# Performance work log

Measured on AMD Instinct MI355X. Metric: run time of the kernel, lower is better.

Reference implementation:

```python
import jax, jax.numpy as jnp
import numpy as np

N_NODES = 50000
N_EDGES = 600000
D = 128  # input_nf = output_nf = hidden_nf
EDGE_IN = 2 * D + 1   # source, target, radial
NODE_IN = 2 * D       # x, agg


def _glorot(key, shape):
    fan_in, fan_out = shape[0], shape[1]
    lim = float(np.sqrt(6.0 / (fan_in + fan_out)))
    return jax.random.uniform(key, shape, jnp.float32, -lim, lim)


def setup_inputs() -> dict:
    key = jax.random.key(0)
    ks = jax.random.split(key, 16)
    h = jax.random.normal(ks[0], (N_NODES, D), jnp.float32)
    edge_index = jax.random.randint(ks[1], (2, N_EDGES), 0, N_NODES, jnp.int64 if jax.config.read('jax_enable_x64') else jnp.int32)
    coord = jax.random.uniform(ks[2], (N_NODES, 3), jnp.float32)
    l = jnp.array([10.0, 10.0, 10.0], jnp.float32)  # periodic box lengths (non-trainable buffer)
    return {
        'h': h, 'edge_index': edge_index, 'coord': coord, 'num_nodes': N_NODES, 'l': l,
        # edge_mlp: Linear(257,128) SiLU Linear(128,128) SiLU
        'We1': _glorot(ks[3], (EDGE_IN, D)), 'be1': jnp.zeros((D,), jnp.float32),
        'We2': _glorot(ks[4], (D, D)),       'be2': jnp.zeros((D,), jnp.float32),
        # node_mlp: Linear(256,128) SiLU Linear(128,128)
        'Wn1': _glorot(ks[5], (NODE_IN, D)), 'bn1': jnp.zeros((D,), jnp.float32),
        'Wn2': _glorot(ks[6], (D, D)),       'bn2': jnp.zeros((D,), jnp.float32),
        # coord_mlp: Linear(128,128) SiLU Linear(128,1, bias=False, xavier gain=0.001)
        'Wc1': _glorot(ks[7], (D, D)),       'bc1': jnp.zeros((D,), jnp.float32),
        'Wc2': _glorot(ks[8], (D, 1)) * 0.001,
    }


def reference(h, edge_index, coord, num_nodes, l,
              We1, be1, We2, be2, Wn1, bn1, Wn2, bn2, Wc1, bc1, Wc2):
    row, col = edge_index[0], edge_index[1]

    # coord2radial with periodic minimum-image wrap
    diff = coord[row] - coord[col]                       # [E, 3]
    diff = jnp.where(diff > 0.5 * l, diff - l, diff)
    diff = jnp.where(diff < -0.5 * l, diff + l, diff)
    radial = jnp.sum(diff * diff, axis=1, keepdims=True)  # [E, 1]

    # edge model: gather -> concat -> 2-layer SiLU MLP
    eh = jnp.concatenate([h[row], h[col], radial], axis=1)  # [E, 257]
    eh = jax.nn.silu(eh @ We1 + be1)
    edge_feat = jax.nn.silu(eh @ We2 + be2)                 # [E, 128]

    # coord model: trans/agg computed in the original but discarded (dead code);
    # only the periodic remainder of coord is returned.
    coord_out = jnp.remainder(coord, l)

    # node model: scatter-add edge features into nodes, then MLP + residual
    agg = jax.ops.segment_sum(edge_feat, row, num_segments=num_nodes)  # [N, 128]
    nh = jnp.concatenate([h, agg], axis=1)                              # [N, 256]
    nh = jax.nn.silu(nh @ Wn1 + bn1)
    h_out = h + (nh @ Wn2 + bn2)

    return h_out, coord_out, edge_feat
```

## Files before the change

### kernel.cpp

```cpp
#include <hip/hip_runtime.h>
#include <math.h>

#define D 128
#define SXS 264
#define SHS 132
#define SFS 132

typedef unsigned int u32;
typedef unsigned short u16;
typedef __attribute__((ext_vector_type(8))) short bf16x8;
typedef __attribute__((ext_vector_type(4))) float f32x4;
typedef __attribute__((ext_vector_type(2))) float f32x2;

__device__ __forceinline__ float bfl(u32 u) { return __uint_as_float(u << 16); }
__device__ __forceinline__ float bfh(u32 u) { return __uint_as_float(u & 0xFFFF0000u); }
__device__ __forceinline__ u16 f2bf(float f) {
    u32 u = __float_as_uint(f);
    return (u16)((u + 0x7FFFu + ((u >> 16) & 1u)) >> 16);
}
__device__ __forceinline__ u32 cvt_pk_bf16(float lo, float hi) {
    u32 r;
    asm("v_cvt_pk_bf16_f32 %0, %1, %2" : "=v"(r) : "v"(lo), "v"(hi));
    return r;
}
__device__ __forceinline__ u16 cvt1_bf16(float v) { return (u16)cvt_pk_bf16(v, v); }
__device__ __forceinline__ float silu_f(float x) {
    float e = __expf(-x);
    return x * __builtin_amdgcn_rcpf(1.0f + e);
}
__device__ __forceinline__ void atomic_pk_add_bf16(u16* addr, u32 pk) {
    asm volatile("global_atomic_pk_add_bf16 %0, %1, off sc1"
                 :: "v"(addr), "v"(pk) : "memory");
}

__global__ void coord_kernel(const float* __restrict__ coord,
                             const float* __restrict__ lbox,
                             float* __restrict__ out, int n3) {
    int i = blockIdx.x * 256 + threadIdx.x;
    if (i < n3) {
        float ld = lbox[i % 3];
        float c = coord[i];
        float r = fmodf(c, ld);
        if (r < 0.f) r += ld;
        out[i] = r;
    }
}

__global__ __launch_bounds__(256) void prep_plus_kernel(
    const float* __restrict__ We1, const float* __restrict__ We2,
    const float* __restrict__ Wn1, const float* __restrict__ Wn2,
    u16* __restrict__ wt,
    int* __restrict__ cursor, int N,
    u16* __restrict__ agg16, long agg_n,
    int* __restrict__ bstate,
    int B1, int B2, int B3)
{
    const int b = blockIdx.x, t = threadIdx.x;
    if (b < B1) {
        int i = b * 256 + t;
        if (i < 32768)        { int n = i >> 8, k = i & 255;              wt[i] = f2bf(We1[(size_t)k*D + n]); }
        else if (i < 49152)   { int j = i - 32768; int n = j >> 7, k = j & 127; wt[i] = f2bf(We2[(size_t)k*D + n]); }
        else if (i < 81920)   { int j = i - 49152; int n = j >> 8, k = j & 255; wt[i] = f2bf(Wn1[(size_t)k*D + n]); }
        else                  { int j = i - 81920; int n = j >> 7, k = j & 127; wt[i] = f2bf(Wn2[(size_t)k*D + n]); }
    } else if (b < B2) {
        int i = ((b - B1) * 256 + t) * 4;
        if (i + 3 < N) *(int4*)(cursor + i) = make_int4(0, 0, 0, 0);
        else for (int k = 0; k < 4; ++k) if (i + k < N) cursor[i + k] = 0;
    } else if (b < B3) {
        long i = ((long)(b - B2) * 256 + t) * 8;
        if (agg16 && i < agg_n) *(uint4*)(agg16 + i) = make_uint4(0, 0, 0, 0);
    } else {
        if (t < 64) bstate[t] = 0;
    }
}

__global__ void hist4_kernel(const int* __restrict__ ei, int* __restrict__ cnt, int E) {
    int i = (blockIdx.x * 256 + threadIdx.x) * 4;
    if (i + 3 < E) {
        int4 r = *(const int4*)(ei + i);
        atomicAdd(&cnt[r.x], 1); atomicAdd(&cnt[r.y], 1);
        atomicAdd(&cnt[r.z], 1); atomicAdd(&cnt[r.w], 1);
    } else {
        for (int k = 0; k < 4; ++k) if (i + k < E) atomicAdd(&cnt[ei[i + k]], 1);
    }
}

__global__ __launch_bounds__(256) void scan_lb_kernel(int* __restrict__ cursor,
                                                      int* __restrict__ bstate, int n) {
    __shared__ int s[256];
    __shared__ int sExcl;
    const int t = threadIdx.x, b = blockIdx.x;
    const int base = b * 1024 + t * 4;
    int v[4];
    #pragma unroll
    for (int i = 0; i < 4; ++i) { int idx = base + i; v[i] = (idx < n - 1) ? cursor[idx] : 0; }
    int lsum = v[0] + v[1] + v[2] + v[3];
    s[t] = lsum; __syncthreads();
    #pragma unroll
    for (int off = 1; off < 256; off <<= 1) {
        int x = (t >= off) ? s[t - off] : 0; __syncthreads();
        s[t] += x; __syncthreads();
    }
    if (t == 0)
        __hip_atomic_store(&bstate[b], 0x40000000 | s[255], __ATOMIC_RELEASE, __HIP_MEMORY_SCOPE_AGENT);
    if (t < 64) {
        int val = 0;
        if (t < b) {
            int st;
            do { st = __hip_atomic_load(&bstate[t], __ATOMIC_ACQUIRE, __HIP_MEMORY_SCOPE_AGENT); }
            while (!(st & 0x40000000));
            val = st & 0x3FFFFFFF;
        }
        #pragma unroll
        for (int off = 1; off < 64; off <<= 1) val += __shfl_xor(val, off, 64);
        if (t == 0) sExcl = val;
    }
    __syncthreads();
    int run = sExcl + s[t] - lsum;
    #pragma unroll
    for (int i = 0; i < 4; ++i) {
        int idx = base + i;
        if (idx < n - 1) cursor[idx] = run;
        run += v[i];
    }
}

__global__ void scan1_kernel(const int* __restrict__ cnt, int* __restrict__ offs,
                             int* __restrict__ bsum, int n) {
    __shared__ int s[256];
    int t = threadIdx.x, b = blockIdx.x;
    int base = b * 1024 + t * 4;
    int v[4];
    #pragma unroll
    for (int i = 0; i < 4; ++i) { int idx = base + i; v[i] = (idx < n - 1) ? cnt[idx] : 0; }
    int lsum = v[0] + v[1] + v[2] + v[3];
    s[t] = lsum; __syncthreads();
    #pragma unroll
    for (int off = 1; off < 256; off <<= 1) {
        int x = (t >= off) ? s[t - off] : 0; __syncthreads();
        s[t] += x; __syncthreads();
    }
    int run = s[t] - lsum;
    #pragma unroll
    for (int i = 0; i < 4; ++i) { int idx = base + i; if (idx < n) offs[idx] = run; run += v[i]; }
    if (t == 255) bsum[b] = s[255];
}

__global__ void scan2_kernel(int* __restrict__ bsum, int nb) {
    __shared__ int s[64];
    int t = threadIdx.x;
    int orig = (t < nb) ? bsum[t] : 0;
    s[t] = orig; __syncthreads();
    #pragma unroll
    for (int off = 1; off < 64; off <<= 1) {
        int x = (t >= off) ? s[t - off] : 0; __syncthreads();
        s[t] += x; __syncthreads();
    }
    if (t < nb) bsum[t] = s[t] - orig;
}

__global__ void scan3_kernel(int* __restrict__ offs, const int* __restrict__ bsum,
                             int* __restrict__ cursor, int n) {
    int i = blockIdx.x * 256 + threadIdx.x;
    if (i < n) {
        int v = offs[i] + bsum[i >> 10];
        offs[i] = v;
        if (i < n - 1) cursor[i] = v;
    }
}

__global__ void scatter4_kernel(const int* __restrict__ ei, int* __restrict__ cursor,
                                int* __restrict__ perm, int4* __restrict__ edata, int E) {
    int i = (blockIdx.x * 256 + threadIdx.x) * 4;
    if (i + 3 < E) {
        int4 r = *(const int4*)(ei + i);
        int4 c = *(const int4*)(ei + (size_t)E + i);
        int p0 = atomicAdd(&cursor[r.x], 1);
        int p1 = atomicAdd(&cursor[r.y], 1);
        int p2 = atomicAdd(&cursor[r.z], 1);
        int p3 = atomicAdd(&cursor[r.w], 1);
        if (edata) {
            edata[p0] = make_int4(i,     r.x, c.x, 0);
            edata[p1] = make_int4(i + 1, r.y, c.y, 0);
            edata[p2] = make_int4(i + 2, r.z, c.z, 0);
            edata[p3] = make_int4(i + 3, r.w, c.w, 0);
        } else {
            perm[p0] = i; perm[p1] = i + 1; perm[p2] = i + 2; perm[p3] = i + 3;
        }
    } else {
        for (int k = 0; k < 4; ++k) {
            int e = i + k;
            if (e < E) {
                int r = ei[e], c = ei[(size_t)E + e];
                int p = atomicAdd(&cursor[r], 1);
                if (edata) edata[p] = make_int4(e, r, c, 0);
                else perm[p] = e;
            }
        }
    }
}

__global__ __launch_bounds__(256, 4) void pq_kernel(
    const float* __restrict__ h, const u16* __restrict__ wt,
    const float* __restrict__ be1,
    u16* __restrict__ Pt, u16* __restrict__ Qt, int N,
    const float* __restrict__ coord, const float* __restrict__ lbox,
    float* __restrict__ coord_out, int n3, int NBn)
{
    __shared__ __align__(16) u16 sA[64 * SHS];
    __shared__ __align__(16) u16 sO[64 * SHS];

    const int t = threadIdx.x;

    if (blockIdx.x >= NBn) {
        int i = (blockIdx.x - NBn) * 256 + t;
        if (i < n3) {
            float ld = lbox[i % 3];
            float c = coord[i];
            float r = fmodf(c, ld);
            if (r < 0.f) r += ld;
            coord_out[i] = r;
        }
        return;
    }

    const int lane = t & 63;
    const int wid = t >> 6;
    const int n0 = blockIdx.x * 64;

    {
        const int e = t & 63, q = t >> 6;
        int ng = n0 + e; int ns = (ng < N) ? ng : N - 1;
        const float4* src = (const float4*)(h + (size_t)ns * D + q * 32);
        u16* dst = sA + e * SHS + q * 32;
        #pragma unroll
        for (int c = 0; c < 4; ++c) {
            float4 a = src[2 * c], b = src[2 * c + 1];
            *(uint4*)(dst + c * 8) = make_uint4(cvt_pk_bf16(a.x, a.y), cvt_pk_bf16(a.z, a.w),
                                               cvt_pk_bf16(b.x, b.y), cvt_pk_bf16(b.z, b.w));
        }
    }
    __syncthreads();

    const int lrow = lane & 15;
    const int kg = lane >> 4;
    const int g4 = kg * 4;
    const int nbase = wid * 32;

    f32x4 accP[4][2] = {}, accQ[4][2] = {};
    {
        bf16x8 Bt[8], Bm[8];
        #pragma unroll
        for (int nn = 0; nn < 2; ++nn)
            #pragma unroll
            for (int s = 0; s < 4; ++s) {
                const u16* bp = wt + (size_t)(nbase + nn * 16 + lrow) * 256 + s * 32 + kg * 8;
                Bt[nn * 4 + s] = *(const bf16x8*)bp;
                Bm[nn * 4 + s] = *(const bf16x8*)(bp + 128);
            }
        #pragma unroll
        for (int s = 0; s < 4; ++s) {
            bf16x8 a[4];
            #pragma unroll
            for (int m = 0; m < 4; ++m)
                a[m] = *(const bf16x8*)(sA + (m * 16 + lrow) * SHS + s * 32 + kg * 8);
            #pragma unroll
            for (int m = 0; m < 4; ++m)
                #pragma unroll
                for (int nn = 0; nn < 2; ++nn) {
                    accP[m][nn] = __builtin_amdgcn_mfma_f32_16x16x32_bf16(a[m], Bt[nn * 4 + s], accP[m][nn], 0, 0, 0);
                    accQ[m][nn] = __builtin_amdgcn_mfma_f32_16x16x32_bf16(a[m], Bm[nn * 4 + s], accQ[m][nn], 0, 0, 0);
                }
        }
    }

    #pragma unroll
    for (int nn = 0; nn < 2; ++nn) {
        int outc = nbase + nn * 16 + lrow;
        float bb = be1[outc];
        #pragma unroll
        for (int m = 0; m < 4; ++m)
            #pragma unroll
            for (int r = 0; r < 4; ++r)
                sO[(m * 16 + g4 + r) * SHS + outc] = cvt1_bf16(accP[m][nn][r] + bb);
    }
    __syncthreads();
    {
        const int f4 = t & 15, rb = t >> 4;
        #pragma unroll
        for (int p = 0; p < 4; ++p) {
            int row = rb + p * 16;
            int ng = n0 + row;
            if (ng < N)
                *(uint4*)(Pt + (size_t)ng * D + f4 * 8) = *(const uint4*)(sO + row * SHS + f4 * 8);
        }
    }
    __syncthreads();
    #pragma unroll
    for (int nn = 0; nn < 2; ++nn) {
        int outc = nbase + nn * 16 + lrow;
        #pragma unroll
        for (int m = 0; m < 4; ++m)
            #pragma unroll
            for (int r = 0; r < 4; ++r)
                sO[(m * 16 + g4 + r) * SHS + outc] = cvt1_bf16(accQ[m][nn][r]);
    }
    __syncthreads();
    {
        const int f4 = t & 15, rb = t >> 4;
        #pragma unroll
        for (int p = 0; p < 4; ++p) {
            int row = rb + p * 16;
            int ng = n0 + row;
            if (ng < N)
                *(uint4*)(Qt + (size_t)ng * D + f4 * 8) = *(const uint4*)(sO + row * SHS + f4 * 8);
        }
    }
}

__global__ __launch_bounds__(256, 8) void edge_pq_kernel(
    const u16* __restrict__ Pt, const u16* __restrict__ Qt,
    const int* __restrict__ ei, const int* __restrict__ perm,
    const int4* __restrict__ edata,
    const float* __restrict__ coord, const float* __restrict__ lbox,
    const u16* __restrict__ wt, const float* __restrict__ We1,
    const float* __restrict__ be2,
    float* __restrict__ ef_out, float* __restrict__ aggf,
    u16* __restrict__ agg16, int E)
{
    __shared__ __align__(16) u16 uni[64 * SHS];
    __shared__ int srow[64], scol[64], sEid[64];
    __shared__ float sRad[64];
    __shared__ float sW[128];
    u16* sH1 = uni;
    u16* sE16 = uni;

    const int t = threadIdx.x;
    const int lane = t & 63;
    const int wid = t >> 6;

    int p0;
    {
        const int nwg = gridDim.x;
        const int orig = blockIdx.x;
        const int q = nwg >> 3, r = nwg & 7;
        const int xcd = orig & 7, idx = orig >> 3;
        const int tile = (xcd < r ? xcd * (q + 1) : r * (q + 1) + (xcd - r) * q) + idx;
        p0 = tile * 64;
    }

    if (t < 64) {
        int slot = p0 + t;
        bool valid = slot < E;
        int cs = valid ? slot : (E - 1);
        int eg, rr, cc;
        if (edata) {
            int4 ed = edata[cs];
            eg = ed.x; rr = ed.y; cc = ed.z;
        } else {
            eg = perm[cs];
            rr = ei[eg];
            cc = ei[(size_t)E + eg];
        }
        sEid[t] = valid ? eg : -1;
        srow[t] = rr;
        scol[t] = cc;
        float rad = 0.f;
        #pragma unroll
        for (int d3 = 0; d3 < 3; ++d3) {
            float df = coord[(size_t)rr * 3 + d3] - coord[(size_t)cc * 3 + d3];
            float ld = lbox[d3];
            df = (df >  0.5f * ld) ? df - ld : df;
            df = (df < -0.5f * ld) ? df + ld : df;
            rad += df * df;
        }
        sRad[t] = rad;
    } else if (t < 192) {
        sW[t - 64] = We1[(size_t)256 * D + (t - 64)];
    }
    __syncthreads();

    {
        const int e = t & 63, q = t >> 6;
        const u16* Pp = Pt + (size_t)srow[e] * D;
        const u16* Qp = Qt + (size_t)scol[e] * D;
        const float rad = sRad[e];
        #pragma unroll
        for (int c0 = 0; c0 < 4; ++c0) {
            int j0 = q * 32 + c0 * 8;
            uint4 pu = *(const uint4*)(Pp + j0);
            uint4 qu = *(const uint4*)(Qp + j0);
            u32 pa[4] = {pu.x, pu.y, pu.z, pu.w};
            u32 qa[4] = {qu.x, qu.y, qu.z, qu.w};
            u32 ow[4];
            #pragma unroll
            for (int k = 0; k < 4; ++k) {
                float w0 = sW[j0 + 2 * k], w1 = sW[j0 + 2 * k + 1];
                float v0 = silu_f(bfl(pa[k]) + bfl(qa[k]) + rad * w0);
                float v1 = silu_f(bfh(pa[k]) + bfh(qa[k]) + rad * w1);
                ow[k] = cvt_pk_bf16(v0, v1);
            }
            *(uint4*)(sH1 + e * SHS + j0) = make_uint4(ow[0], ow[1], ow[2], ow[3]);
        }
    }
    __syncthreads();

    const int lrow = lane & 15;
    const int kg = lane >> 4;
    const int g4 = kg * 4;
    const int nbase = wid * 32;

    f32x4 acc2[4][2] = {};
    {
        bf16x8 B2[8];
        #pragma unroll
        for (int nn = 0; nn < 2; ++nn)
            #pragma unroll
            for (int s = 0; s < 4; ++s)
                B2[nn * 4 + s] = *(const bf16x8*)(wt + 32768 + (size_t)(nbase + nn * 16 + lrow) * 128 + s * 32 + kg * 8);
        #pragma unroll
        for (int s = 0; s < 4; ++s) {
            bf16x8 a[4];
            #pragma unroll
            for (int m = 0; m < 4; ++m)
                a[m] = *(const bf16x8*)(sH1 + (m * 16 + lrow) * SHS + s * 32 + kg * 8);
            #pragma unroll
            for (int m = 0; m < 4; ++m)
                #pragma unroll
                for (int nn = 0; nn < 2; ++nn)
                    acc2[m][nn] = __builtin_amdgcn_mfma_f32_16x16x32_bf16(a[m], B2[nn * 4 + s], acc2[m][nn], 0, 0, 0);
        }
    }
    __syncthreads();

    #pragma unroll
    for (int nn = 0; nn < 2; ++nn) {
        int outc = nbase + nn * 16 + lrow;
        float bb = be2[outc];
        #pragma unroll
        for (int m = 0; m < 4; ++m)
            #pragma unroll
            for (int r = 0; r < 4; ++r)
                sE16[(m * 16 + g4 + r) * SHS + outc] = cvt1_bf16(silu_f(acc2[m][nn][r] + bb));
    }
    __syncthreads();

    if (agg16) {
        const int cp = t & 63;
        const int g = t >> 6;
        const int ebeg = g * 16, eend = ebeg + 16;
        float r0 = 0.f, r1 = 0.f;
        int prev = srow[ebeg];
        for (int e = ebeg; e < eend; ++e) {
            int r = srow[e];
            if (r != prev) {
                if (r0 != 0.f || r1 != 0.f)
                    atomic_pk_add_bf16(agg16 + (size_t)prev * D + 2 * cp, cvt_pk_bf16(r0, r1));
                r0 = 0.f; r1 = 0.f; prev = r;
            }
            int eg = sEid[e];
            if (eg >= 0) {
                u32 pk2 = *(const u32*)(sE16 + e * SHS + 2 * cp);
                float v0 = bfl(pk2), v1 = bfh(pk2);
                f32x2 vv = {v0, v1};
                __builtin_nontemporal_store(vv, (f32x2*)&ef_out[(size_t)eg * D + 2 * cp]);
                r0 += v0; r1 += v1;
            }
        }
        if (r0 != 0.f || r1 != 0.f)
            atomic_pk_add_bf16(agg16 + (size_t)prev * D + 2 * cp, cvt_pk_bf16(r0, r1));
    } else {
        const int ct = t & 127;
        const int half = t >> 7;
        const int ebeg = half * 32, eend = ebeg + 32;
        float run = 0.f;
        int prev = srow[ebeg];
        for (int e = ebeg; e < eend; ++e) {
            int r = srow[e];
            if (r != prev) {
                if (run != 0.f) atomicAdd(&aggf[(size_t)prev * D + ct], run);
                run = 0.f; prev = r;
            }
            int eg = sEid[e];
            if (eg >= 0) {
                float v = __uint_as_float((u32)sE16[e * SHS + ct] << 16);
                __builtin_nontemporal_store(v, &ef_out[(size_t)eg * D + ct]);
                run += v;
            }
        }
        if (run != 0.f) atomicAdd(&aggf[(size_t)prev * D + ct], run);
    }
}

__global__ __launch_bounds__(256, 3) void edge_fb_kernel(
    const float* __restrict__ h,
    const int* __restrict__ ei, const int* __restrict__ perm,
    const float* __restrict__ coord, const float* __restrict__ lbox,
    const u16* __restrict__ wt,
    const float* __restrict__ We1, const float* __restrict__ be1,
    const float* __restrict__ be2,
    float* __restrict__ ef_out, float* __restrict__ aggf, int E)
{
    __shared__ __align__(16) u16 sX[64 * SXS];
    __shared__ __align__(16) u16 sH1[64 * SHS];
    __shared__ int srow[64], scol[64], sEid[64];
    __shared__ float sRad[64];

    const int t = threadIdx.x;
    const int lane = t & 63;
    const int wid = t >> 6;

    int p0;
    {
        const int nwg = gridDim.x;
        const int orig = blockIdx.x;
        const int q = nwg >> 3, r = nwg & 7;
        const int xcd = orig & 7, idx = orig >> 3;
        const int tile = (xcd < r ? xcd * (q + 1) : r * (q + 1) + (xcd - r) * q) + idx;
        p0 = tile * 64;
    }

    if (t < 64) {
        int slot = p0 + t;
        int eg = perm[(slot < E) ? slot : (E - 1)];
        sEid[t] = (p0 + t < E) ? eg : -1;
        srow[t] = ei[eg];
        scol[t] = ei[(size_t)E + eg];
    }
    __syncthreads();

    {
        const int e = t & 63;
        const int q = t >> 6;
        const int r = srow[e], c = scol[e];
        const float4* src = (const float4*)((q < 2) ? (h + (size_t)r * D + (q & 1) * 64)
                                                    : (h + (size_t)c * D + (q & 1) * 64));
        u16* dst = sX + e * SXS + q * 64;
        #pragma unroll
        for (int i = 0; i < 8; ++i) {
            float4 a = src[2 * i], b = src[2 * i + 1];
            *(uint4*)(dst + i * 8) = make_uint4(cvt_pk_bf16(a.x, a.y), cvt_pk_bf16(a.z, a.w),
                                               cvt_pk_bf16(b.x, b.y), cvt_pk_bf16(b.z, b.w));
        }
        if (t < 64) {
            int rr = srow[t], cc = scol[t];
            float rad = 0.f;
            #pragma unroll
            for (int d3 = 0; d3 < 3; ++d3) {
                float df = coord[(size_t)rr * 3 + d3] - coord[(size_t)cc * 3 + d3];
                float ld = lbox[d3];
                df = (df >  0.5f * ld) ? df - ld : df;
                df = (df < -0.5f * ld) ? df + ld : df;
                rad += df * df;
            }
            sRad[t] = rad;
        }
    }
    __syncthreads();

    const int lrow = lane & 15;
    const int kg = lane >> 4;
    const int g4 = kg * 4;
    const int nbase = wid * 32;

    f32x4 acc[4][2] = {};
    {
        bf16x8 B1[16];
        #pragma unroll
        for (int nn = 0; nn < 2; ++nn)
            #pragma unroll
            for (int s = 0; s < 8; ++s)
                B1[nn * 8 + s] = *(const bf16x8*)(wt + (size_t)(nbase + nn * 16 + lrow) * 256 + s * 32 + kg * 8);
        #pragma unroll
        for (int s = 0; s < 8; ++s) {
            bf16x8 a[4];
            #pragma unroll
            for (int m = 0; m < 4; ++m)
                a[m] = *(const bf16x8*)(sX + (m * 16 + lrow) * SXS + s * 32 + kg * 8);
            #pragma unroll
            for (int m = 0; m < 4; ++m)
                #pragma unroll
                for (int nn = 0; nn < 2; ++nn)
                    acc[m][nn] = __builtin_amdgcn_mfma_f32_16x16x32_bf16(a[m], B1[nn * 8 + s], acc[m][nn], 0, 0, 0);
        }
    }

    #pragma unroll
    for (int nn = 0; nn < 2; ++nn) {
        int outc = nbase + nn * 16 + lrow;
        float wl = We1[(size_t)256 * D + outc];
        float bb = be1[outc];
        #pragma unroll
        for (int m = 0; m < 4; ++m)
            #pragma unroll
            for (int r = 0; r < 4; ++r) {
                int e = m * 16 + g4 + r;
                float v = acc[m][nn][r] + sRad[e] * wl + bb;
                sH1[e * SHS + outc] = cvt1_bf16(silu_f(v));
            }
    }
    __syncthreads();

    f32x4 acc2[4][2] = {};
    {
        bf16x8 B2[8];
        #pragma unroll
        for (int nn = 0; nn < 2; ++nn)
            #pragma unroll
            for (int s = 0; s < 4; ++s)
                B2[nn * 4 + s] = *(const bf16x8*)(wt + 32768 + (size_t)(nbase + nn * 16 + lrow) * 128 + s * 32 + kg * 8);
        #pragma unroll
        for (int s = 0; s < 4; ++s) {
            bf16x8 a[4];
            #pragma unroll
            for (int m = 0; m < 4; ++m)
                a[m] = *(const bf16x8*)(sH1 + (m * 16 + lrow) * SHS + s * 32 + kg * 8);
            #pragma unroll
            for (int m = 0; m < 4; ++m)
                #pragma unroll
                for (int nn = 0; nn < 2; ++nn)
                    acc2[m][nn] = __builtin_amdgcn_mfma_f32_16x16x32_bf16(a[m], B2[nn * 4 + s], acc2[m][nn], 0, 0, 0);
        }
    }
    __syncthreads();

    float* sXf = (float*)sX;
    #pragma unroll
    for (int nn = 0; nn < 2; ++nn) {
        int outc = nbase + nn * 16 + lrow;
        float bb = be2[outc];
        #pragma unroll
        for (int m = 0; m < 4; ++m)
            #pragma unroll
            for (int r = 0; r < 4; ++r)
                sXf[(m * 16 + g4 + r) * SFS + outc] = silu_f(acc2[m][nn][r] + bb);
    }
    __syncthreads();

    {
        const int ct = t & 127;
        const int half = t >> 7;
        const int ebeg = half * 32, eend = ebeg + 32;
        float run = 0.f;
        int prev = srow[ebeg];
        for (int e = ebeg; e < eend; ++e) {
            int r = srow[e];
            if (r != prev) {
                if (run != 0.f) atomicAdd(&aggf[(size_t)prev * D + ct], run);
                run = 0.f; prev = r;
            }
            int eg = sEid[e];
            if (eg >= 0) {
                float v = sXf[e * SFS + ct];
                __builtin_nontemporal_store(v, &ef_out[(size_t)eg * D + ct]);
                run += v;
            }
        }
        if (run != 0.f) atomicAdd(&aggf[(size_t)prev * D + ct], run);
    }
}

__global__ __launch_bounds__(256, 4) void node_kernel(
    const float* __restrict__ h, const float* __restrict__ aggf,
    const u16* __restrict__ agg16,
    const u16* __restrict__ wt,
    const float* __restrict__ bn1, const float* __restrict__ bn2,
    float* __restrict__ h_out, int N)
{
    __shared__ __align__(16) u16 uni[64 * SXS];
    u16* sX = uni;
    u16* sH1 = uni;
    float* sXf = (float*)uni;

    const int t = threadIdx.x;
    const int lane = t & 63;
    const int wid = t >> 6;
    const int n0 = blockIdx.x * 64;

    {
        const int e = t & 63;
        const int q = t >> 6;
        int ng = n0 + e; int ns = (ng < N) ? ng : N - 1;
        u16* dst = sX + e * SXS + q * 64;
        if (q >= 2 && agg16) {
            const u16* src = agg16 + (size_t)ns * D + (q & 1) * 64;
            #pragma unroll
            for (int i = 0; i < 8; ++i)
                *(uint4*)(dst + i * 8) = *(const uint4*)(src + i * 8);
        } else {
            const float4* src = (const float4*)(((q < 2) ? h : aggf) + (size_t)ns * D + (q & 1) * 64);
            #pragma unroll
            for (int i = 0; i < 8; ++i) {
                float4 a = src[2 * i], b = src[2 * i + 1];
                *(uint4*)(dst + i * 8) = make_uint4(cvt_pk_bf16(a.x, a.y), cvt_pk_bf16(a.z, a.w),
                                                   cvt_pk_bf16(b.x, b.y), cvt_pk_bf16(b.z, b.w));
            }
        }
    }
    __syncthreads();

    const int lrow = lane & 15;
    const int kg = lane >> 4;
    const int g4 = kg * 4;
    const int nbase = wid * 32;

    f32x4 acc[4][2] = {};
    {
        bf16x8 B1[16];
        #pragma unroll
        for (int nn = 0; nn < 2; ++nn)
            #pragma unroll
            for (int s = 0; s < 8; ++s)
                B1[nn * 8 + s] = *(const bf16x8*)(wt + 49152 + (size_t)(nbase + nn * 16 + lrow) * 256 + s * 32 + kg * 8);
        #pragma unroll
        for (int s = 0; s < 8; ++s) {
            bf16x8 a[4];
            #pragma unroll
            for (int m = 0; m < 4; ++m)
                a[m] = *(const bf16x8*)(sX + (m * 16 + lrow) * SXS + s * 32 + kg * 8);
            #pragma unroll
            for (int m = 0; m < 4; ++m)
                #pragma unroll
                for (int nn = 0; nn < 2; ++nn)
                    acc[m][nn] = __builtin_amdgcn_mfma_f32_16x16x32_bf16(a[m], B1[nn * 8 + s], acc[m][nn], 0, 0, 0);
        }
    }
    __syncthreads();

    #pragma unroll
    for (int nn = 0; nn < 2; ++nn) {
        int outc = nbase + nn * 16 + lrow;
        float bb = bn1[outc];
        #pragma unroll
        for (int m = 0; m < 4; ++m)
            #pragma unroll
            for (int r = 0; r < 4; ++r)
                sH1[(m * 16 + g4 + r) * SHS + outc] = cvt1_bf16(silu_f(acc[m][nn][r] + bb));
    }
    __syncthreads();

    f32x4 acc2[4][2] = {};
    {
        bf16x8 B2[8];
        #pragma unroll
        for (int nn = 0; nn < 2; ++nn)
            #pragma unroll
            for (int s = 0; s < 4; ++s)
                B2[nn * 4 + s] = *(const bf16x8*)(wt + 81920 + (size_t)(nbase + nn * 16 + lrow) * 128 + s * 32 + kg * 8);
        #pragma unroll
        for (int s = 0; s < 4; ++s) {
            bf16x8 a[4];
            #pragma unroll
            for (int m = 0; m < 4; ++m)
                a[m] = *(const bf16x8*)(sH1 + (m * 16 + lrow) * SHS + s * 32 + kg * 8);
            #pragma unroll
            for (int m = 0; m < 4; ++m)
                #pragma unroll
                for (int nn = 0; nn < 2; ++nn)
                    acc2[m][nn] = __builtin_amdgcn_mfma_f32_16x16x32_bf16(a[m], B2[nn * 4 + s], acc2[m][nn], 0, 0, 0);
        }
    }
    __syncthreads();

    #pragma unroll
    for (int nn = 0; nn < 2; ++nn) {
        int outc = nbase + nn * 16 + lrow;
        float bb = bn2[outc];
        #pragma unroll
        for (int m = 0; m < 4; ++m)
            #pragma unroll
            for (int r = 0; r < 4; ++r)
                sXf[(m * 16 + g4 + r) * SFS + outc] = acc2[m][nn][r] + bb;
    }
    __syncthreads();

    {
        const int f4 = t & 31;
        const int nb = t >> 5;
        #pragma unroll
        for (int i = 0; i < 8; ++i) {
            int nl = nb + i * 8;
            int ng = n0 + nl;
            if (ng < N) {
                f32x4 v = *(const f32x4*)&sXf[nl * SFS + f4 * 4];
                const f32x4 hv = *(const f32x4*)&h[(size_t)ng * D + f4 * 4];
                v += hv;
                __builtin_nontemporal_store(v, (f32x4*)&h_out[(size_t)ng * D + f4 * 4]);
            }
        }
    }
}

extern "C" void kernel_launch(void* const* d_in, const int* in_sizes, int n_in,
                              void* d_out, int out_size, void* d_ws, size_t ws_size,
                              hipStream_t stream) {
    const float* h     = (const float*)d_in[0];
    const int*   ei    = (const int*)d_in[1];
    const float* coord = (const float*)d_in[2];
    const float* lbox  = (const float*)d_in[4];
    const float* We1   = (const float*)d_in[5];
    const float* be1   = (const float*)d_in[6];
    const float* We2   = (const float*)d_in[7];
    const float* be2   = (const float*)d_in[8];
    const float* Wn1   = (const float*)d_in[9];
    const float* bn1   = (const float*)d_in[10];
    const float* Wn2   = (const float*)d_in[11];
    const float* bn2   = (const float*)d_in[12];

    const int N = in_sizes[0] / D;
    const int E = in_sizes[1] / 2;

    float* out       = (float*)d_out;
    float* h_out     = out;
    float* coord_out = out + (size_t)N * D;
    float* ef_out    = coord_out + (size_t)N * 3;
    float* aggf      = h_out;

    int* wsi = (int*)d_ws;
    u16* wt     = (u16*)d_ws;
    int* offs   = wsi + 49152;
    int* cursor = offs + (N + 8);
    int* bsum   = cursor + (N + 8);
    int* perm   = bsum + 64;
    u16* Pt     = (u16*)(perm + E);
    u16* Qt     = Pt + (size_t)N * D;
    int4* edata = (int4*)(((uintptr_t)(Qt + (size_t)N * D) + 15) & ~(uintptr_t)15);
    u16* agg16  = (u16*)(edata + E);

    size_t need_pq  = (size_t)((char*)(Qt + (size_t)N * D) - (char*)d_ws);
    size_t need_ed  = (size_t)((char*)(edata + E) - (char*)d_ws);
    size_t need_a16 = (size_t)((char*)(agg16 + (size_t)N * D) - (char*)d_ws);
    const bool use_pq  = ws_size >= need_pq;
    const bool use_ed  = use_pq && ws_size >= need_ed;
    const bool use_a16 = use_ed && ws_size >= need_a16;
    int4* edp  = use_ed ? edata : nullptr;
    u16*  a16p = use_a16 ? agg16 : nullptr;

    const int nb1 = (N + 1 + 1023) / 1024;
    const bool lbscan = nb1 <= 64;

    const long agg_n = (long)N * D;
    const int B1 = 384;
    const int B2 = B1 + (N / 4 + 255) / 256;
    const int B3 = B2 + (use_a16 ? (int)((agg_n / 8 + 255) / 256) : 0);
    const int Bt = B3 + 1;
    prep_plus_kernel<<<Bt, 256, 0, stream>>>(We1, We2, Wn1, Wn2, wt,
                                             cursor, N, a16p, agg_n, bsum, B1, B2, B3);

    if (use_pq) {
        const int NBn = (N + 63) / 64;
        const int NBc = (N * 3 + 255) / 256;
        pq_kernel<<<NBn + NBc, 256, 0, stream>>>(h, wt, be1, Pt, Qt, N,
                                                 coord, lbox, coord_out, N * 3, NBn);
    } else {
        coord_kernel<<<(N * 3 + 255) / 256, 256, 0, stream>>>(coord, lbox, coord_out, N * 3);
    }

    if (!use_a16)
        hipMemsetAsync(aggf, 0, (size_t)N * D * sizeof(float), stream);

    hist4_kernel<<<(E / 4 + 255) / 256, 256, 0, stream>>>(ei, cursor, E);
    if (lbscan) {
        scan_lb_kernel<<<nb1, 256, 0, stream>>>(cursor, bsum, N + 1);
    } else {
        scan1_kernel<<<nb1, 256, 0, stream>>>(cursor, offs, bsum, N + 1);
        scan2_kernel<<<1, 64, 0, stream>>>(bsum, nb1);
        scan3_kernel<<<(N + 1 + 255) / 256, 256, 0, stream>>>(offs, bsum, cursor, N + 1);
    }
    scatter4_kernel<<<(E / 4 + 255) / 256, 256, 0, stream>>>(ei, cursor, perm, edp, E);

    if (use_pq)
        edge_pq_kernel<<<(E + 63) / 64, 256, 0, stream>>>(
            Pt, Qt, ei, perm, edp, coord, lbox, wt, We1, be2, ef_out, aggf, a16p, E);
    else
        edge_fb_kernel<<<(E + 63) / 64, 256, 0, stream>>>(
            h, ei, perm, coord, lbox, wt, We1, be1, be2, ef_out, aggf, E);

    node_kernel<<<(N + 63) / 64, 256, 0, stream>>>(
        h, aggf, a16p, wt, bn1, bn2, h_out, N);
}
```

Before: 241.8 us.

## Fuse histogram into pq kernel and fuse scan with scatter via grid barrier

The edge-row histogram now runs as extra blocks of the pq_kernel launch instead of its own kernel. The decoupled-lookback scan and the edge scatter are merged into one kernel, with a global atomic counter acting as a barrier between them. This removes two kernel launches and their gaps from the serial prep chain. The barrier has every block spin until all scan blocks finish, which assumes the scan blocks get scheduled; the scatter grid is about 586 blocks, small enough to fit on the device at once.

```diff
diff --git a/kernel.cpp b/kernel.cpp
--- a/kernel.cpp
+++ b/kernel.cpp
@@ -70,7 +70,7 @@
         long i = ((long)(b - B2) * 256 + t) * 8;
         if (agg16 && i < agg_n) *(uint4*)(agg16 + i) = make_uint4(0, 0, 0, 0);
     } else {
-        if (t < 64) bstate[t] = 0;
+        if (t < 80) bstate[t] = 0;
     }
 }
 
@@ -82,46 +82,6 @@
         atomicAdd(&cnt[r.z], 1); atomicAdd(&cnt[r.w], 1);
     } else {
         for (int k = 0; k < 4; ++k) if (i + k < E) atomicAdd(&cnt[ei[i + k]], 1);
-    }
-}
-
-__global__ __launch_bounds__(256) void scan_lb_kernel(int* __restrict__ cursor,
-                                                      int* __restrict__ bstate, int n) {
-    __shared__ int s[256];
-    __shared__ int sExcl;
-    const int t = threadIdx.x, b = blockIdx.x;
-    const int base = b * 1024 + t * 4;
-    int v[4];
-    #pragma unroll
-    for (int i = 0; i < 4; ++i) { int idx = base + i; v[i] = (idx < n - 1) ? cursor[idx] : 0; }
-    int lsum = v[0] + v[1] + v[2] + v[3];
-    s[t] = lsum; __syncthreads();
-    #pragma unroll
-    for (int off = 1; off < 256; off <<= 1) {
-        int x = (t >= off) ? s[t - off] : 0; __syncthreads();
-        s[t] += x; __syncthreads();
-    }
-    if (t == 0)
-        __hip_atomic_store(&bstate[b], 0x40000000 | s[255], __ATOMIC_RELEASE, __HIP_MEMORY_SCOPE_AGENT);
-    if (t < 64) {
-        int val = 0;
-        if (t < b) {
-            int st;
-            do { st = __hip_atomic_load(&bstate[t], __ATOMIC_ACQUIRE, __HIP_MEMORY_SCOPE_AGENT); }
-            while (!(st & 0x40000000));
-            val = st & 0x3FFFFFFF;
-        }
-        #pragma unroll
-        for (int off = 1; off < 64; off <<= 1) val += __shfl_xor(val, off, 64);
-        if (t == 0) sExcl = val;
-    }
-    __syncthreads();
-    int run = sExcl + s[t] - lsum;
-    #pragma unroll
-    for (int i = 0; i < 4; ++i) {
-        int idx = base + i;
-        if (idx < n - 1) cursor[idx] = run;
-        run += v[i];
     }
 }
 
@@ -200,18 +160,118 @@
     }
 }
 
+__global__ __launch_bounds__(256) void scan_scatter_kernel(
+    int* __restrict__ cursor, int* __restrict__ bstate, int n , int nb1,
+    const int* __restrict__ ei, int* __restrict__ perm, int4* __restrict__ edata,
+    int E, int G)
+{
+    __shared__ int s[256];
+    __shared__ int sExcl;
+    const int t = threadIdx.x, b = blockIdx.x;
+
+    if (b < nb1) {
+        const int base = b * 1024 + t * 4;
+        int v[4];
+        #pragma unroll
+        for (int i = 0; i < 4; ++i) { int idx = base + i; v[i] = (idx < n - 1) ? cursor[idx] : 0; }
+        int lsum = v[0] + v[1] + v[2] + v[3];
+        s[t] = lsum; __syncthreads();
+        #pragma unroll
+        for (int off = 1; off < 256; off <<= 1) {
+            int x = (t >= off) ? s[t - off] : 0; __syncthreads();
+            s[t] += x; __syncthreads();
+        }
+        if (t == 0)
+            __hip_atomic_store(&bstate[b], 0x40000000 | s[255], __ATOMIC_RELEASE, __HIP_MEMORY_SCOPE_AGENT);
+        if (t < 64) {
+            int val = 0;
+            if (t < b) {
+                int st;
+                do { st = __hip_atomic_load(&bstate[t], __ATOMIC_ACQUIRE, __HIP_MEMORY_SCOPE_AGENT); }
+                while (!(st & 0x40000000));
+                val = st & 0x3FFFFFFF;
+            }
+            #pragma unroll
+            for (int off = 1; off < 64; off <<= 1) val += __shfl_xor(val, off, 64);
+            if (t == 0) sExcl = val;
+        }
+        __syncthreads();
+        int run = sExcl + s[t] - lsum;
+        #pragma unroll
+        for (int i = 0; i < 4; ++i) {
+            int idx = base + i;
+            if (idx < n - 1) cursor[idx] = run;
+            run += v[i];
+        }
+        __syncthreads();
+        __threadfence();
+        if (t == 0)
+            __hip_atomic_fetch_add(&bstate[64], 1, __ATOMIC_RELEASE, __HIP_MEMORY_SCOPE_AGENT);
+    }
+
+    if (t == 0) {
+        int v;
+        do { v = __hip_atomic_load(&bstate[64], __ATOMIC_ACQUIRE, __HIP_MEMORY_SCOPE_AGENT); }
+        while (v < nb1);
+    }
+    __syncthreads();
+
+    const int nquad = (E + 3) / 4;
+    for (int qi = b * 256 + t; qi < nquad; qi += G * 256) {
+        int i = qi * 4;
+        if (i + 3 < E) {
+            int4 r = *(const int4*)(ei + i);
+            int4 c = *(const int4*)(ei + (size_t)E + i);
+            int p0 = atomicAdd(&cursor[r.x], 1);
+            int p1 = atomicAdd(&cursor[r.y], 1);
+            int p2 = atomicAdd(&cursor[r.z], 1);
+            int p3 = atomicAdd(&cursor[r.w], 1);
+            if (edata) {
+                edata[p0] = make_int4(i,     r.x, c.x, 0);
+                edata[p1] = make_int4(i + 1, r.y, c.y, 0);
+                edata[p2] = make_int4(i + 2, r.z, c.z, 0);
+                edata[p3] = make_int4(i + 3, r.w, c.w, 0);
+            } else {
+                perm[p0] = i; perm[p1] = i + 1; perm[p2] = i + 2; perm[p3] = i + 3;
+            }
+        } else {
+            for (int k = 0; k < 4; ++k) {
+                int e = i + k;
+                if (e < E) {
+                    int r = ei[e], c = ei[(size_t)E + e];
+                    int p = atomicAdd(&cursor[r], 1);
+                    if (edata) edata[p] = make_int4(e, r, c, 0);
+                    else perm[p] = e;
+                }
+            }
+        }
+    }
+}
+
 __global__ __launch_bounds__(256, 4) void pq_kernel(
     const float* __restrict__ h, const u16* __restrict__ wt,
     const float* __restrict__ be1,
     u16* __restrict__ Pt, u16* __restrict__ Qt, int N,
     const float* __restrict__ coord, const float* __restrict__ lbox,
-    float* __restrict__ coord_out, int n3, int NBn)
+    float* __restrict__ coord_out, int n3, int NBn, int NBc,
+    const int* __restrict__ ei, int* __restrict__ cursor, int E)
 {
     __shared__ __align__(16) u16 sA[64 * SHS];
     __shared__ __align__(16) u16 sO[64 * SHS];
 
     const int t = threadIdx.x;
 
+    if (blockIdx.x >= NBn + NBc) {
+        int i = ((blockIdx.x - NBn - NBc) * 256 + t) * 4;
+        if (i + 3 < E) {
+            int4 r = *(const int4*)(ei + i);
+            atomicAdd(&cursor[r.x], 1); atomicAdd(&cursor[r.y], 1);
+            atomicAdd(&cursor[r.z], 1); atomicAdd(&cursor[r.w], 1);
+        } else {
+            for (int k = 0; k < 4; ++k) if (i + k < E) atomicAdd(&cursor[ei[i + k]], 1);
+        }
+        return;
+    }
     if (blockIdx.x >= NBn) {
         int i = (blockIdx.x - NBn) * 256 + t;
         if (i < n3) {
@@ -253,23 +313,23 @@
         #pragma unroll
         for (int nn = 0; nn < 2; ++nn)
             #pragma unroll
-            for (int s = 0; s < 4; ++s) {
-                const u16* bp = wt + (size_t)(nbase + nn * 16 + lrow) * 256 + s * 32 + kg * 8;
-                Bt[nn * 4 + s] = *(const bf16x8*)bp;
-                Bm[nn * 4 + s] = *(const bf16x8*)(bp + 128);
-            }
-        #pragma unroll
-        for (int s = 0; s < 4; ++s) {
+            for (int s2 = 0; s2 < 4; ++s2) {
+                const u16* bp = wt + (size_t)(nbase + nn * 16 + lrow) * 256 + s2 * 32 + kg * 8;
+                Bt[nn * 4 + s2] = *(const bf16x8*)bp;
+                Bm[nn * 4 + s2] = *(const bf16x8*)(bp + 128);
+            }
+        #pragma unroll
+        for (int s2 = 0; s2 < 4; ++s2) {
             bf16x8 a[4];
             #pragma unroll
             for (int m = 0; m < 4; ++m)
-                a[m] = *(const bf16x8*)(sA + (m * 16 + lrow) * SHS + s * 32 + kg * 8);
+                a[m] = *(const bf16x8*)(sA + (m * 16 + lrow) * SHS + s2 * 32 + kg * 8);
             #pragma unroll
             for (int m = 0; m < 4; ++m)
                 #pragma unroll
                 for (int nn = 0; nn < 2; ++nn) {
-                    accP[m][nn] = __builtin_amdgcn_mfma_f32_16x16x32_bf16(a[m], Bt[nn * 4 + s], accP[m][nn], 0, 0, 0);
-                    accQ[m][nn] = __builtin_amdgcn_mfma_f32_16x16x32_bf16(a[m], Bm[nn * 4 + s], accQ[m][nn], 0, 0, 0);
+                    accP[m][nn] = __builtin_amdgcn_mfma_f32_16x16x32_bf16(a[m], Bt[nn * 4 + s2], accP[m][nn], 0, 0, 0);
+                    accQ[m][nn] = __builtin_amdgcn_mfma_f32_16x16x32_bf16(a[m], Bm[nn * 4 + s2], accQ[m][nn], 0, 0, 0);
                 }
         }
     }
@@ -416,19 +476,19 @@
         #pragma unroll
         for (int nn = 0; nn < 2; ++nn)
             #pragma unroll
-            for (int s = 0; s < 4; ++s)
-                B2[nn * 4 + s] = *(const bf16x8*)(wt + 32768 + (size_t)(nbase + nn * 16 + lrow) * 128 + s * 32 + kg * 8);
-        #pragma unroll
-        for (int s = 0; s < 4; ++s) {
+            for (int s2 = 0; s2 < 4; ++s2)
+                B2[nn * 4 + s2] = *(const bf16x8*)(wt + 32768 + (size_t)(nbase + nn * 16 + lrow) * 128 + s2 * 32 + kg * 8);
+        #pragma unroll
+        for (int s2 = 0; s2 < 4; ++s2) {
             bf16x8 a[4];
             #pragma unroll
             for (int m = 0; m < 4; ++m)
-                a[m] = *(const bf16x8*)(sH1 + (m * 16 + lrow) * SHS + s * 32 + kg * 8);
+                a[m] = *(const bf16x8*)(sH1 + (m * 16 + lrow) * SHS + s2 * 32 + kg * 8);
             #pragma unroll
             for (int m = 0; m < 4; ++m)
                 #pragma unroll
                 for (int nn = 0; nn < 2; ++nn)
-                    acc2[m][nn] = __builtin_amdgcn_mfma_f32_16x16x32_bf16(a[m], B2[nn * 4 + s], acc2[m][nn], 0, 0, 0);
+                    acc2[m][nn] = __builtin_amdgcn_mfma_f32_16x16x32_bf16(a[m], B2[nn * 4 + s2], acc2[m][nn], 0, 0, 0);
         }
     }
     __syncthreads();
@@ -569,19 +629,19 @@
         #pragma unroll
         for (int nn = 0; nn < 2; ++nn)
             #pragma unroll
-            for (int s = 0; s < 8; ++s)
-                B1[nn * 8 + s] = *(const bf16x8*)(wt + (size_t)(nbase + nn * 16 + lrow) * 256 + s * 32 + kg * 8);
-        #pragma unroll
-        for (int s = 0; s < 8; ++s) {
+            for (int s2 = 0; s2 < 8; ++s2)
+                B1[nn * 8 + s2] = *(const bf16x8*)(wt + (size_t)(nbase + nn * 16 + lrow) * 256 + s2 * 32 + kg * 8);
+        #pragma unroll
+        for (int s2 = 0; s2 < 8; ++s2) {
             bf16x8 a[4];
             #pragma unroll
             for (int m = 0; m < 4; ++m)
-                a[m] = *(const bf16x8*)(sX + (m * 16 + lrow) * SXS + s * 32 + kg * 8);
+                a[m] = *(const bf16x8*)(sX + (m * 16 + lrow) * SXS + s2 * 32 + kg * 8);
             #pragma unroll
             for (int m = 0; m < 4; ++m)
                 #pragma unroll
                 for (int nn = 0; nn < 2; ++nn)
-                    acc[m][nn] = __builtin_amdgcn_mfma_f32_16x16x32_bf16(a[m], B1[nn * 8 + s], acc[m][nn], 0, 0, 0);
+                    acc[m][nn] = __builtin_amdgcn_mfma_f32_16x16x32_bf16(a[m], B1[nn * 8 + s2], acc[m][nn], 0, 0, 0);
         }
     }
 
@@ -607,19 +667,19 @@
         #pragma unroll
         for (int nn = 0; nn < 2; ++nn)
             #pragma unroll
-            for (int s = 0; s < 4; ++s)
-                B2[nn * 4 + s] = *(const bf16x8*)(wt + 32768 + (size_t)(nbase + nn * 16 + lrow) * 128 + s * 32 + kg * 8);
-        #pragma unroll
-        for (int s = 0; s < 4; ++s) {
+            for (int s2 = 0; s2 < 4; ++s2)
+                B2[nn * 4 + s2] = *(const bf16x8*)(wt + 32768 + (size_t)(nbase + nn * 16 + lrow) * 128 + s2 * 32 + kg * 8);
+        #pragma unroll
+        for (int s2 = 0; s2 < 4; ++s2) {
             bf16x8 a[4];
             #pragma unroll
             for (int m = 0; m < 4; ++m)
-                a[m] = *(const bf16x8*)(sH1 + (m * 16 + lrow) * SHS + s * 32 + kg * 8);
+                a[m] = *(const bf16x8*)(sH1 + (m * 16 + lrow) * SHS + s2 * 32 + kg * 8);
             #pragma unroll
             for (int m = 0; m < 4; ++m)
                 #pragma unroll
                 for (int nn = 0; nn < 2; ++nn)
-                    acc2[m][nn] = __builtin_amdgcn_mfma_f32_16x16x32_bf16(a[m], B2[nn * 4 + s], acc2[m][nn], 0, 0, 0);
+                    acc2[m][nn] = __builtin_amdgcn_mfma_f32_16x16x32_bf16(a[m], B2[nn * 4 + s2], acc2[m][nn], 0, 0, 0);
         }
     }
     __syncthreads();
@@ -710,19 +770,19 @@
         #pragma unroll
         for (int nn = 0; nn < 2; ++nn)
             #pragma unroll
-            for (int s = 0; s < 8; ++s)
-                B1[nn * 8 + s] = *(const bf16x8*)(wt + 49152 + (size_t)(nbase + nn * 16 + lrow) * 256 + s * 32 + kg * 8);
-        #pragma unroll
-        for (int s = 0; s < 8; ++s) {
+            for (int s2 = 0; s2 < 8; ++s2)
+                B1[nn * 8 + s2] = *(const bf16x8*)(wt + 49152 + (size_t)(nbase + nn * 16 + lrow) * 256 + s2 * 32 + kg * 8);
+        #pragma unroll
+        for (int s2 = 0; s2 < 8; ++s2) {
             bf16x8 a[4];
             #pragma unroll
             for (int m = 0; m < 4; ++m)
-                a[m] = *(const bf16x8*)(sX + (m * 16 + lrow) * SXS + s * 32 + kg * 8);
+                a[m] = *(const bf16x8*)(sX + (m * 16 + lrow) * SXS + s2 * 32 + kg * 8);
             #pragma unroll
             for (int m = 0; m < 4; ++m)
                 #pragma unroll
                 for (int nn = 0; nn < 2; ++nn)
-                    acc[m][nn] = __builtin_amdgcn_mfma_f32_16x16x32_bf16(a[m], B1[nn * 8 + s], acc[m][nn], 0, 0, 0);
+                    acc[m][nn] = __builtin_amdgcn_mfma_f32_16x16x32_bf16(a[m], B1[nn * 8 + s2], acc[m][nn], 0, 0, 0);
         }
     }
     __syncthreads();
@@ -745,19 +805,19 @@
         #pragma unroll
         for (int nn = 0; nn < 2; ++nn)
             #pragma unroll
-            for (int s = 0; s < 4; ++s)
-                B2[nn * 4 + s] = *(const bf16x8*)(wt + 81920 + (size_t)(nbase + nn * 16 + lrow) * 128 + s * 32 + kg * 8);
-        #pragma unroll
-        for (int s = 0; s < 4; ++s) {
+            for (int s2 = 0; s2 < 4; ++s2)
+                B2[nn * 4 + s2] = *(const bf16x8*)(wt + 81920 + (size_t)(nbase + nn * 16 + lrow) * 128 + s2 * 32 + kg * 8);
+        #pragma unroll
+        for (int s2 = 0; s2 < 4; ++s2) {
             bf16x8 a[4];
             #pragma unroll
             for (int m = 0; m < 4; ++m)
-                a[m] = *(const bf16x8*)(sH1 + (m * 16 + lrow) * SHS + s * 32 + kg * 8);
+                a[m] = *(const bf16x8*)(sH1 + (m * 16 + lrow) * SHS + s2 * 32 + kg * 8);
             #pragma unroll
             for (int m = 0; m < 4; ++m)
                 #pragma unroll
                 for (int nn = 0; nn < 2; ++nn)
-                    acc2[m][nn] = __builtin_amdgcn_mfma_f32_16x16x32_bf16(a[m], B2[nn * 4 + s], acc2[m][nn], 0, 0, 0);
+                    acc2[m][nn] = __builtin_amdgcn_mfma_f32_16x16x32_bf16(a[m], B2[nn * 4 + s2], acc2[m][nn], 0, 0, 0);
         }
     }
     __syncthreads();
@@ -820,8 +880,8 @@
     u16* wt     = (u16*)d_ws;
     int* offs   = wsi + 49152;
     int* cursor = offs + (N + 8);
-    int* bsum   = cursor + (N + 8);
-    int* perm   = bsum + 64;
+    int* bstate = cursor + (N + 8);
+    int* perm   = bstate + 80;
     u16* Pt     = (u16*)(perm + E);
     u16* Qt     = Pt + (size_t)N * D;
     int4* edata = (int4*)(((uintptr_t)(Qt + (size_t)N * D) + 15) & ~(uintptr_t)15);
@@ -838,6 +898,7 @@
 
     const int nb1 = (N + 1 + 1023) / 1024;
     const bool lbscan = nb1 <= 64;
+    const int nqb = (E / 4 + 255) / 256;
 
     const long agg_n = (long)N * D;
     const int B1 = 384;
@@ -845,29 +906,32 @@
     const int B3 = B2 + (use_a16 ? (int)((agg_n / 8 + 255) / 256) : 0);
     const int Bt = B3 + 1;
     prep_plus_kernel<<<Bt, 256, 0, stream>>>(We1, We2, Wn1, Wn2, wt,
-                                             cursor, N, a16p, agg_n, bsum, B1, B2, B3);
+                                             cursor, N, a16p, agg_n, bstate, B1, B2, B3);
 
     if (use_pq) {
         const int NBn = (N + 63) / 64;
         const int NBc = (N * 3 + 255) / 256;
-        pq_kernel<<<NBn + NBc, 256, 0, stream>>>(h, wt, be1, Pt, Qt, N,
-                                                 coord, lbox, coord_out, N * 3, NBn);
+        pq_kernel<<<NBn + NBc + nqb, 256, 0, stream>>>(h, wt, be1, Pt, Qt, N,
+                                                       coord, lbox, coord_out, N * 3, NBn, NBc,
+                                                       ei, cursor, E);
     } else {
         coord_kernel<<<(N * 3 + 255) / 256, 256, 0, stream>>>(coord, lbox, coord_out, N * 3);
+        hist4_kernel<<<nqb, 256, 0, stream>>>(ei, cursor, E);
     }
 
     if (!use_a16)
         hipMemsetAsync(aggf, 0, (size_t)N * D * sizeof(float), stream);
 
-    hist4_kernel<<<(E / 4 + 255) / 256, 256, 0, stream>>>(ei, cursor, E);
     if (lbscan) {
-        scan_lb_kernel<<<nb1, 256, 0, stream>>>(cursor, bsum, N + 1);
+        const int G = nqb < nb1 ? nb1 : nqb;
+        scan_scatter_kernel<<<G, 256, 0, stream>>>(cursor, bstate, N + 1, nb1,
+                                                   ei, perm, edp, E, G);
     } else {
-        scan1_kernel<<<nb1, 256, 0, stream>>>(cursor, offs, bsum, N + 1);
-        scan2_kernel<<<1, 64, 0, stream>>>(bsum, nb1);
-        scan3_kernel<<<(N + 1 + 255) / 256, 256, 0, stream>>>(offs, bsum, cursor, N + 1);
-    }
-    scatter4_kernel<<<(E / 4 + 255) / 256, 256, 0, stream>>>(ei, cursor, perm, edp, E);
+        scan1_kernel<<<nb1, 256, 0, stream>>>(cursor, offs, bstate, N + 1);
+        scan2_kernel<<<1, 64, 0, stream>>>(bstate, nb1);
+        scan3_kernel<<<(N + 1 + 255) / 256, 256, 0, stream>>>(offs, bstate, cursor, N + 1);
+        scatter4_kernel<<<nqb, 256, 0, stream>>>(ei, cursor, perm, edp, E);
+    }
 
     if (use_pq)
         edge_pq_kernel<<<(E + 63) / 64, 256, 0, stream>>>(
```

Result: slower. 272.5 us (+12.7%).
